# Kernel tuning notes

Hardware: AMD Instinct MI355X
Metric: run time of the kernel (lower is better)

Reference implementation:

```python
import jax, jax.numpy as jnp
import numpy as np

H = 4096        # hidden_size
NH = 32         # num query heads
NKV = 8         # num kv heads
HD = H // NH    # head_dim = 128
T_PREV = 16383  # cached tokens; new token makes T = 16384
BASE = 10000.0


def _rope(x, pos):
    # x: [heads, head_dim]; interleaved even/odd RoPE at a single position
    d = x.shape[-1]
    inv_freq = 1.0 / (BASE ** (jnp.arange(0, d, 2, dtype=jnp.float32) / d))
    f = pos * inv_freq                      # [d/2]
    c, s = jnp.cos(f), jnp.sin(f)
    xe, xo = x[..., 0::2], x[..., 1::2]
    out = jnp.stack([xe * c - xo * s, xe * s + xo * c], axis=-1)
    return out.reshape(x.shape)


def setup_inputs() -> dict:
    key = jax.random.key(0)
    ks = jax.random.split(key, 7)
    w = 0.02  # weight scale for numerical stability
    return {
        "hidden": jax.random.normal(ks[0], (H,), jnp.float32),
        "k_cache": jax.random.normal(ks[1], (T_PREV, NKV, HD), jnp.float32),
        "v_cache": jax.random.normal(ks[2], (T_PREV, NKV, HD), jnp.float32),
        "Wq": jax.random.normal(ks[3], (H, H), jnp.float32) * w,
        "Wk": jax.random.normal(ks[4], (NKV * HD, H), jnp.float32) * w,
        "Wv": jax.random.normal(ks[5], (NKV * HD, H), jnp.float32) * w,
        "Wo": jax.random.normal(ks[6], (H, H), jnp.float32) * w,
        "position_id": T_PREV,
    }


def reference(hidden, k_cache, v_cache, Wq, Wk, Wv, Wo, position_id):
    pos = jnp.float32(position_id)
    # projections (nn.Linear: y = W @ x), single token
    q = (Wq @ hidden).reshape(NH, HD)
    k = (Wk @ hidden).reshape(NKV, HD)
    v = (Wv @ hidden).reshape(NKV, HD)
    # inline RoPE on new q and k
    q = _rope(q, pos)
    k = _rope(k, pos)
    # contiguous KV including the new token
    k_all = jnp.concatenate([k_cache, k[None]], axis=0)   # [T, NKV, HD]
    v_all = jnp.concatenate([v_cache, v[None]], axis=0)
    # GQA: repeat KV heads to match query heads
    rep = NH // NKV
    k_all = jnp.repeat(k_all, rep, axis=1)                 # [T, NH, HD]
    v_all = jnp.repeat(v_all, rep, axis=1)
    # single-query attention
    scores = jnp.einsum('hd,thd->ht', q, k_all) / jnp.sqrt(jnp.float32(HD))
    attn = jax.nn.softmax(scores, axis=-1)                 # [NH, T]
    ctx = jnp.einsum('ht,thd->hd', attn, v_all)            # [NH, HD]
    # combine heads + output projection
    return Wo @ ctx.reshape(H)
```

## Files before the change

### kernel.cpp

```cpp
#include <hip/hip_runtime.h>
#include <math.h>
#include <stdint.h>

#define NH 32
#define NKV 8
#define HD 128
#define HDIM 4096
#define KVDIM 1024
#define TPREV 16383
#define NCHUNK 128
#define CHUNK 128
#define PTOK 64

#define OFF_Q 0
#define OFF_K 4096
#define OFF_V 5120
#define OFF_PART 6144
#define PART_STRIDE 132
#define OFF_CTX (OFF_PART + NH * NCHUNK * PART_STRIDE)

__device__ __forceinline__ float wave_reduce_sum(float v) {
#pragma unroll
  for (int m = 32; m >= 1; m >>= 1) v += __shfl_xor(v, m, 64);
  return v;
}
__device__ __forceinline__ float wave_reduce_max(float v) {
#pragma unroll
  for (int m = 32; m >= 1; m >>= 1) v = fmaxf(v, __shfl_xor(v, m, 64));
  return v;
}
__device__ __forceinline__ float dot4(float4 a, float4 b) {
  return a.x * b.x + a.y * b.y + a.z * b.z + a.w * b.w;
}

typedef const __attribute__((address_space(1))) unsigned int* gld_gp;
typedef __attribute__((address_space(3))) unsigned int* gld_lp;
__device__ __forceinline__ void cp16(const float* g, float* l) {
  __builtin_amdgcn_global_load_lds((gld_gp)(uintptr_t)g,
                                   (gld_lp)(uint32_t)(uintptr_t)l, 16, 0, 0);
}

#define BAR_LGKM()                                       \
  do {                                                   \
    asm volatile("s_waitcnt lgkmcnt(0)" ::: "memory");   \
    __builtin_amdgcn_s_barrier();                        \
    asm volatile("" ::: "memory");                       \
  } while (0)

__global__ __launch_bounds__(256) void qkv_rope_kernel(
    const float* __restrict__ Wq, const float* __restrict__ Wk,
    const float* __restrict__ Wv, const float* __restrict__ hidden,
    const int* __restrict__ pos_p, float* __restrict__ ws) {
  int r = blockIdx.x * 4 + (threadIdx.x >> 6);
  int lane = threadIdx.x & 63;
  const float* W;
  int wr;
  if (r < HDIM) {
    W = Wq; wr = r;
  } else if (r < HDIM + KVDIM) {
    W = Wk; wr = r - HDIM;
  } else {
    W = Wv; wr = r - HDIM - KVDIM;
  }
  const float4* w4 = (const float4*)(W + (size_t)wr * HDIM);
  const float4* h4 = (const float4*)hidden;
  float s = 0.f;
#pragma unroll
  for (int base = 0; base < 16; base += 8) {
    float4 a[8], b[8];
#pragma unroll
    for (int j = 0; j < 8; ++j) a[j] = w4[lane + 64 * (base + j)];
#pragma unroll
    for (int j = 0; j < 8; ++j) b[j] = h4[lane + 64 * (base + j)];
#pragma unroll
    for (int j = 0; j < 8; ++j) s += dot4(a[j], b[j]);
  }
  s = wave_reduce_sum(s);
  __shared__ float rs[4];
  if (lane == 0) rs[threadIdx.x >> 6] = s;
  __syncthreads();
  if (threadIdx.x < 2) {
    int r0 = blockIdx.x * 4 + (int)threadIdx.x * 2;
    float S0 = rs[threadIdx.x * 2], S1 = rs[threadIdx.x * 2 + 1];
    if (r0 < HDIM + KVDIM) {
      int j = (r0 & (HD - 1)) >> 1;
      double lowp = 1.0;
      if (j & 1) lowp *= 0.8659643233600653;
      if (j & 2) lowp *= 0.7498942093324559;
      if (j & 4) lowp *= 0.5623413251903491;
      if (j & 8) lowp *= 0.31622776601683794;
      double hi = (j & 16) ? 0.1 : 1.0;
      if (j & 32) hi *= 0.01;
      double f = (double)(*pos_p) * (lowp * hi);
      double k2 = floor(f * 0.15915494309189535);
      double rr = f - k2 * 6.283185307179586;
      float fr = (float)rr;
      float c = cosf(fr), sn = sinf(fr);
      ws[r0] = S0 * c - S1 * sn;
      ws[r0 + 1] = S0 * sn + S1 * c;
    } else {
      ws[r0] = S0;
      ws[r0 + 1] = S1;
    }
  }
}

__global__ __launch_bounds__(256, 2) void attn_chunk_kernel(
    const float* __restrict__ k_cache, const float* __restrict__ v_cache,
    float* __restrict__ ws) {
  int g = blockIdx.x >> 7;
  int c = blockIdx.x & 127;
  int t0 = c * CHUNK;
  int tid = threadIdx.x;
  int l = tid & 63, w = tid >> 6;

  __shared__ __align__(16) float Klds[PTOK * HD];
  __shared__ __align__(16) float Vlds[PTOK * HD];
  __shared__ __align__(16) float qs[4 * HD];
  __shared__ float sc[PTOK * 5];
  __shared__ float rm[4], rl[4], wold[4];
  __shared__ float wredm[4][4], wredl[4][4];

  if (tid < 4) { rm[tid] = -1e30f; rl[tid] = 0.f; }

  if (w < 2)
    cp16(ws + OFF_Q + (g << 9) + (w << 8) + (l << 2), qs + (w << 8));
#pragma unroll
  for (int i = 0; i < 8; ++i) {
    int tokA = (w << 4) + 2 * i;
    int toks = tokA + (l >> 5);
    int gt = t0 + toks;
    if (gt >= TPREV) gt = 0;
    cp16(k_cache + (size_t)gt * KVDIM + g * HD + (((l & 31) ^ (toks & 7)) << 2),
         Klds + (tokA << 7));
  }
#pragma unroll
  for (int i = 0; i < 8; ++i) {
    int tokA = (w << 4) + 2 * i;
    int toks = tokA + (l >> 5);
    int gt = t0 + toks;
    if (gt >= TPREV) gt = 0;
    cp16(v_cache + (size_t)gt * KVDIM + g * HD + ((l & 31) << 2),
         Vlds + (tokA << 7));
  }
  asm volatile("s_waitcnt vmcnt(8) lgkmcnt(0)" ::: "memory");
  __builtin_amdgcn_s_barrier();
  asm volatile("" ::: "memory");

  const float rscale = 0.08838834764831845f;
  int tokl = (w << 4) + (l & 15);
  int qq = l >> 4;
  int t7 = tokl & 7;
  int grp8 = tid >> 5, d4 = tid & 31;
  float4 acc0 = {0, 0, 0, 0}, acc1 = {0, 0, 0, 0};
  float4 acc2 = {0, 0, 0, 0}, acc3 = {0, 0, 0, 0};
  const float4* K4 = (const float4*)Klds;
  const float4* q4 = (const float4*)qs;
  const float4* V4 = (const float4*)Vlds;

#pragma unroll
  for (int p = 0; p < 2; ++p) {
    float s0 = 0.f, s1 = 0.f, s2 = 0.f, s3 = 0.f;
#pragma unroll
    for (int j = 0; j < 8; ++j) {
      float4 kk = K4[(tokl << 5) + (qq << 3) + (j ^ t7)];
      float4 qa = q4[0 * 32 + (qq << 3) + j];
      float4 qb = q4[1 * 32 + (qq << 3) + j];
      float4 qc = q4[2 * 32 + (qq << 3) + j];
      float4 qd_ = q4[3 * 32 + (qq << 3) + j];
      s0 += dot4(kk, qa); s1 += dot4(kk, qb);
      s2 += dot4(kk, qc); s3 += dot4(kk, qd_);
    }
    s0 += __shfl_xor(s0, 16, 64); s0 += __shfl_xor(s0, 32, 64);
    s1 += __shfl_xor(s1, 16, 64); s1 += __shfl_xor(s1, 32, 64);
    s2 += __shfl_xor(s2, 16, 64); s2 += __shfl_xor(s2, 32, 64);
    s3 += __shfl_xor(s3, 16, 64); s3 += __shfl_xor(s3, 32, 64);
    s0 *= rscale; s1 *= rscale; s2 *= rscale; s3 *= rscale;
    if (t0 + p * PTOK + tokl >= TPREV) {
      s0 = -1e30f; s1 = -1e30f; s2 = -1e30f; s3 = -1e30f;
    }

    float m0 = wave_reduce_max(s0), m1 = wave_reduce_max(s1);
    float m2 = wave_reduce_max(s2), m3 = wave_reduce_max(s3);
    if (l == 0) {
      wredm[w][0] = m0; wredm[w][1] = m1; wredm[w][2] = m2; wredm[w][3] = m3;
    }
    BAR_LGKM();
    if (p == 0) {
#pragma unroll
      for (int i = 0; i < 8; ++i) {
        int tokA = (w << 4) + 2 * i;
        int toks = tokA + (l >> 5);
        int gt = t0 + PTOK + toks;
        if (gt >= TPREV) gt = 0;
        cp16(k_cache + (size_t)gt * KVDIM + g * HD +
                 (((l & 31) ^ (toks & 7)) << 2),
             Klds + (tokA << 7));
      }
    }
    if (tid < 4) {
      float mh = fmaxf(fmaxf(wredm[0][tid], wredm[1][tid]),
                       fmaxf(wredm[2][tid], wredm[3][tid]));
      float M = fmaxf(rm[tid], mh);
      wold[tid] = expf(rm[tid] - M);
      rm[tid] = M;
    }
    BAR_LGKM();

    float M0 = rm[0], M1 = rm[1], M2 = rm[2], M3 = rm[3];
    float w0 = wold[0], w1 = wold[1], w2 = wold[2], w3 = wold[3];
    acc0.x *= w0; acc0.y *= w0; acc0.z *= w0; acc0.w *= w0;
    acc1.x *= w1; acc1.y *= w1; acc1.z *= w1; acc1.w *= w1;
    acc2.x *= w2; acc2.y *= w2; acc2.z *= w2; acc2.w *= w2;
    acc3.x *= w3; acc3.y *= w3; acc3.z *= w3; acc3.w *= w3;

    float e0 = expf(s0 - M0), e1 = expf(s1 - M1);
    float e2 = expf(s2 - M2), e3 = expf(s3 - M3);
    if (qq == 0) {
      sc[tokl * 5 + 0] = e0; sc[tokl * 5 + 1] = e1;
      sc[tokl * 5 + 2] = e2; sc[tokl * 5 + 3] = e3;
    }
    float l0 = 0.25f * wave_reduce_sum(e0), l1 = 0.25f * wave_reduce_sum(e1);
    float l2 = 0.25f * wave_reduce_sum(e2), l3 = 0.25f * wave_reduce_sum(e3);
    if (l == 0) {
      wredl[w][0] = l0; wredl[w][1] = l1; wredl[w][2] = l2; wredl[w][3] = l3;
    }
    if (p == 0)
      asm volatile("s_waitcnt vmcnt(8) lgkmcnt(0)" ::: "memory");
    else
      asm volatile("s_waitcnt vmcnt(0) lgkmcnt(0)" ::: "memory");
    __builtin_amdgcn_s_barrier();
    asm volatile("" ::: "memory");
    if (tid < 4)
      rl[tid] = rl[tid] * wold[tid] + wredl[0][tid] + wredl[1][tid] +
                wredl[2][tid] + wredl[3][tid];

#pragma unroll
    for (int t = 0; t < 8; ++t) {
      int tok = (grp8 << 3) + t;
      float4 vv = V4[(tok << 5) + d4];
      float p0_ = sc[tok * 5 + 0], p1_ = sc[tok * 5 + 1];
      float p2_ = sc[tok * 5 + 2], p3_ = sc[tok * 5 + 3];
      acc0.x = fmaf(p0_, vv.x, acc0.x); acc0.y = fmaf(p0_, vv.y, acc0.y);
      acc0.z = fmaf(p0_, vv.z, acc0.z); acc0.w = fmaf(p0_, vv.w, acc0.w);
      acc1.x = fmaf(p1_, vv.x, acc1.x); acc1.y = fmaf(p1_, vv.y, acc1.y);
      acc1.z = fmaf(p1_, vv.z, acc1.z); acc1.w = fmaf(p1_, vv.w, acc1.w);
      acc2.x = fmaf(p2_, vv.x, acc2.x); acc2.y = fmaf(p2_, vv.y, acc2.y);
      acc2.z = fmaf(p2_, vv.z, acc2.z); acc2.w = fmaf(p2_, vv.w, acc2.w);
      acc3.x = fmaf(p3_, vv.x, acc3.x); acc3.y = fmaf(p3_, vv.y, acc3.y);
      acc3.z = fmaf(p3_, vv.z, acc3.z); acc3.w = fmaf(p3_, vv.w, acc3.w);
    }

    if (p == 0) {
      BAR_LGKM();
#pragma unroll
      for (int i = 0; i < 8; ++i) {
        int tokA = (w << 4) + 2 * i;
        int toks = tokA + (l >> 5);
        int gt = t0 + PTOK + toks;
        if (gt >= TPREV) gt = 0;
        cp16(v_cache + (size_t)gt * KVDIM + g * HD + ((l & 31) << 2),
             Vlds + (tokA << 7));
      }
      asm volatile("s_waitcnt vmcnt(8)" ::: "memory");
    }
  }

  float4* vacc4 = (float4*)Klds;
  vacc4[(grp8 * 4 + 0) * 32 + d4] = acc0;
  vacc4[(grp8 * 4 + 1) * 32 + d4] = acc1;
  vacc4[(grp8 * 4 + 2) * 32 + d4] = acc2;
  vacc4[(grp8 * 4 + 3) * 32 + d4] = acc3;
  BAR_LGKM();
  if (tid < 128) {
    int h = tid >> 5, dd = tid & 31;
    float4 s = {0, 0, 0, 0};
#pragma unroll
    for (int g2 = 0; g2 < 8; ++g2) {
      float4 v = vacc4[(g2 * 4 + h) * 32 + dd];
      s.x += v.x; s.y += v.y; s.z += v.z; s.w += v.w;
    }
    float* dst = ws + OFF_PART +
                 ((size_t)(g * 4 + h) * NCHUNK + c) * PART_STRIDE + (dd << 2);
    *(float4*)dst = s;
  }
  if (tid < 4) {
    float* base =
        ws + OFF_PART + ((size_t)(g * 4 + tid) * NCHUNK + c) * PART_STRIDE;
    base[128] = rm[tid];
    base[129] = rl[tid];
  }
}

__global__ __launch_bounds__(256) void combine_kernel(float* __restrict__ ws) {
  int h = blockIdx.x;
  int g = h >> 2;
  int tid = threadIdx.x;
  const float rscale = 0.08838834764831845f;
  const float* ph = ws + OFF_PART + (size_t)h * NCHUNK * PART_STRIDE;

  __shared__ float red[HD];
  __shared__ float wexp[NCHUNK];
  __shared__ float wm[4], wl[4];
  __shared__ float acc2[HD];

  if (tid < HD) red[tid] = ws[OFF_Q + h * HD + tid] * ws[OFF_K + g * HD + tid];
  __syncthreads();
#pragma unroll
  for (int s2 = 64; s2 >= 1; s2 >>= 1) {
    if (tid < s2 && tid + s2 < HD) red[tid] += red[tid + s2];
    __syncthreads();
  }
  float snew = red[0] * rscale;

  float mv = (tid < NCHUNK) ? ph[(size_t)tid * PART_STRIDE + 128] : -1e30f;
  float lv = (tid < NCHUNK) ? ph[(size_t)tid * PART_STRIDE + 129] : 0.f;
  float mw = wave_reduce_max(mv);
  if ((tid & 63) == 0) wm[tid >> 6] = mw;
  __syncthreads();
  float M = fmaxf(fmaxf(fmaxf(wm[0], wm[1]), fmaxf(wm[2], wm[3])), snew);
  float w = expf(mv - M);
  if (tid < NCHUNK) wexp[tid] = w;
  float lw = wave_reduce_sum(lv * w);
  if ((tid & 63) == 0) wl[tid >> 6] = lw;
  __syncthreads();
  float en = expf(snew - M);
  float L = wl[0] + wl[1] + wl[2] + wl[3] + en;

  int half = tid >> 7, d = tid & 127;
  float acc = 0.f;
  int cbeg = half * (NCHUNK / 2);
#pragma unroll 8
  for (int c2 = cbeg; c2 < cbeg + NCHUNK / 2; ++c2)
    acc = fmaf(ph[(size_t)c2 * PART_STRIDE + d], wexp[c2], acc);
  if (half == 0) acc2[d] = acc;
  __syncthreads();
  if (half == 1) acc2[d] += acc;
  __syncthreads();
  if (tid < HD)
    ws[OFF_CTX + h * HD + tid] =
        (acc2[tid] + en * ws[OFF_V + g * HD + tid]) / L;
}

__global__ __launch_bounds__(256) void out_matvec_kernel(
    const float* __restrict__ Wo, const float* __restrict__ ws,
    float* __restrict__ out) {
  int r = blockIdx.x * 4 + (threadIdx.x >> 6);
  int lane = threadIdx.x & 63;
  const float4* w4 = (const float4*)(Wo + (size_t)r * HDIM);
  const float4* x4 = (const float4*)(ws + OFF_CTX);
  float s = 0.f;
#pragma unroll
  for (int base = 0; base < 16; base += 8) {
    float4 a[8], b[8];
#pragma unroll
    for (int j = 0; j < 8; ++j) a[j] = w4[lane + 64 * (base + j)];
#pragma unroll
    for (int j = 0; j < 8; ++j) b[j] = x4[lane + 64 * (base + j)];
#pragma unroll
    for (int j = 0; j < 8; ++j) s += dot4(a[j], b[j]);
  }
  s = wave_reduce_sum(s);
  if (lane == 0) out[r] = s;
}

extern "C" void kernel_launch(void* const* d_in, const int* in_sizes, int n_in,
                              void* d_out, int out_size, void* d_ws,
                              size_t ws_size, hipStream_t stream) {
  const float* hidden = (const float*)d_in[0];
  const float* k_cache = (const float*)d_in[1];
  const float* v_cache = (const float*)d_in[2];
  const float* Wq = (const float*)d_in[3];
  const float* Wk = (const float*)d_in[4];
  const float* Wv = (const float*)d_in[5];
  const float* Wo = (const float*)d_in[6];
  const int* pos = (const int*)d_in[7];
  float* out = (float*)d_out;
  float* ws = (float*)d_ws;

  qkv_rope_kernel<<<(HDIM + 2 * KVDIM) / 4, 256, 0, stream>>>(Wq, Wk, Wv,
                                                              hidden, pos, ws);
  attn_chunk_kernel<<<NKV * NCHUNK, 256, 0, stream>>>(k_cache, v_cache, ws);
  combine_kernel<<<NH, 256, 0, stream>>>(ws);
  out_matvec_kernel<<<HDIM / 4, 256, 0, stream>>>(Wo, ws, out);
}
```

Baseline: 287.1 us.

## Split attention into 64-token chunks with single-pass softmax and direct V loads

Halves the chunk size to 64 tokens and doubles the number of chunk blocks, so each block computes one chunk's scores and softmax in a single pass with no online rescaling or double-buffered K/V. V is now read straight from global memory into registers instead of being staged through LDS, which drops the V shared buffer and raises the occupancy target to 4 blocks per CU. The combine kernel now reads 256 per-chunk partials (one per thread). The trade-off is twice as many partial results to write and combine, and the loss of K/V load overlap inside each block.

```diff
diff --git a/kernel.cpp b/kernel.cpp
--- a/kernel.cpp
+++ b/kernel.cpp
@@ -8,9 +8,8 @@
 #define HDIM 4096
 #define KVDIM 1024
 #define TPREV 16383
-#define NCHUNK 128
-#define CHUNK 128
-#define PTOK 64
+#define NCHUNK 256
+#define CHUNK 64
 
 #define OFF_Q 0
 #define OFF_K 4096
@@ -39,13 +38,6 @@
   __builtin_amdgcn_global_load_lds((gld_gp)(uintptr_t)g,
                                    (gld_lp)(uint32_t)(uintptr_t)l, 16, 0, 0);
 }
-
-#define BAR_LGKM()                                       \
-  do {                                                   \
-    asm volatile("s_waitcnt lgkmcnt(0)" ::: "memory");   \
-    __builtin_amdgcn_s_barrier();                        \
-    asm volatile("" ::: "memory");                       \
-  } while (0)
 
 __global__ __launch_bounds__(256) void qkv_rope_kernel(
     const float* __restrict__ Wq, const float* __restrict__ Wk,
@@ -105,23 +97,19 @@
   }
 }
 
-__global__ __launch_bounds__(256, 2) void attn_chunk_kernel(
+__global__ __launch_bounds__(256, 4) void attn_chunk_kernel(
     const float* __restrict__ k_cache, const float* __restrict__ v_cache,
     float* __restrict__ ws) {
-  int g = blockIdx.x >> 7;
-  int c = blockIdx.x & 127;
+  int g = blockIdx.x >> 8;
+  int c = blockIdx.x & 255;
   int t0 = c * CHUNK;
   int tid = threadIdx.x;
   int l = tid & 63, w = tid >> 6;
 
-  __shared__ __align__(16) float Klds[PTOK * HD];
-  __shared__ __align__(16) float Vlds[PTOK * HD];
+  __shared__ __align__(16) float Klds[CHUNK * HD];
   __shared__ __align__(16) float qs[4 * HD];
-  __shared__ float sc[PTOK * 5];
-  __shared__ float rm[4], rl[4], wold[4];
+  __shared__ float sc[CHUNK * 5];
   __shared__ float wredm[4][4], wredl[4][4];
-
-  if (tid < 4) { rm[tid] = -1e30f; rl[tid] = 0.f; }
 
   if (w < 2)
     cp16(ws + OFF_Q + (g << 9) + (w << 8) + (l << 2), qs + (w << 8));
@@ -134,144 +122,99 @@
     cp16(k_cache + (size_t)gt * KVDIM + g * HD + (((l & 31) ^ (toks & 7)) << 2),
          Klds + (tokA << 7));
   }
-#pragma unroll
-  for (int i = 0; i < 8; ++i) {
-    int tokA = (w << 4) + 2 * i;
-    int toks = tokA + (l >> 5);
-    int gt = t0 + toks;
-    if (gt >= TPREV) gt = 0;
-    cp16(v_cache + (size_t)gt * KVDIM + g * HD + ((l & 31) << 2),
-         Vlds + (tokA << 7));
-  }
-  asm volatile("s_waitcnt vmcnt(8) lgkmcnt(0)" ::: "memory");
-  __builtin_amdgcn_s_barrier();
-  asm volatile("" ::: "memory");
+  __syncthreads();
 
   const float rscale = 0.08838834764831845f;
   int tokl = (w << 4) + (l & 15);
   int qq = l >> 4;
   int t7 = tokl & 7;
-  int grp8 = tid >> 5, d4 = tid & 31;
+  const float4* K4 = (const float4*)Klds;
+  const float4* q4 = (const float4*)qs;
+  float s0 = 0.f, s1 = 0.f, s2 = 0.f, s3 = 0.f;
+#pragma unroll
+  for (int j = 0; j < 8; ++j) {
+    float4 kk = K4[(tokl << 5) + (qq << 3) + (j ^ t7)];
+    float4 qa = q4[0 * 32 + (qq << 3) + j];
+    float4 qb = q4[1 * 32 + (qq << 3) + j];
+    float4 qc = q4[2 * 32 + (qq << 3) + j];
+    float4 qd_ = q4[3 * 32 + (qq << 3) + j];
+    s0 += dot4(kk, qa); s1 += dot4(kk, qb);
+    s2 += dot4(kk, qc); s3 += dot4(kk, qd_);
+  }
+  s0 += __shfl_xor(s0, 16, 64); s0 += __shfl_xor(s0, 32, 64);
+  s1 += __shfl_xor(s1, 16, 64); s1 += __shfl_xor(s1, 32, 64);
+  s2 += __shfl_xor(s2, 16, 64); s2 += __shfl_xor(s2, 32, 64);
+  s3 += __shfl_xor(s3, 16, 64); s3 += __shfl_xor(s3, 32, 64);
+  s0 *= rscale; s1 *= rscale; s2 *= rscale; s3 *= rscale;
+  if (t0 + tokl >= TPREV) {
+    s0 = -1e30f; s1 = -1e30f; s2 = -1e30f; s3 = -1e30f;
+  }
+
+  float m0 = wave_reduce_max(s0), m1 = wave_reduce_max(s1);
+  float m2 = wave_reduce_max(s2), m3 = wave_reduce_max(s3);
+  if (l == 0) {
+    wredm[w][0] = m0; wredm[w][1] = m1; wredm[w][2] = m2; wredm[w][3] = m3;
+  }
+  __syncthreads();
+  float mh0 = fmaxf(fmaxf(wredm[0][0], wredm[1][0]),
+                    fmaxf(wredm[2][0], wredm[3][0]));
+  float mh1 = fmaxf(fmaxf(wredm[0][1], wredm[1][1]),
+                    fmaxf(wredm[2][1], wredm[3][1]));
+  float mh2 = fmaxf(fmaxf(wredm[0][2], wredm[1][2]),
+                    fmaxf(wredm[2][2], wredm[3][2]));
+  float mh3 = fmaxf(fmaxf(wredm[0][3], wredm[1][3]),
+                    fmaxf(wredm[2][3], wredm[3][3]));
+
+  float e0 = expf(s0 - mh0), e1 = expf(s1 - mh1);
+  float e2 = expf(s2 - mh2), e3 = expf(s3 - mh3);
+  if (qq == 0) {
+    sc[tokl * 5 + 0] = e0; sc[tokl * 5 + 1] = e1;
+    sc[tokl * 5 + 2] = e2; sc[tokl * 5 + 3] = e3;
+  }
+  float l0 = 0.25f * wave_reduce_sum(e0), l1 = 0.25f * wave_reduce_sum(e1);
+  float l2 = 0.25f * wave_reduce_sum(e2), l3 = 0.25f * wave_reduce_sum(e3);
+  if (l == 0) {
+    wredl[w][0] = l0; wredl[w][1] = l1; wredl[w][2] = l2; wredl[w][3] = l3;
+  }
+  __syncthreads();
+
+  int grp = tid >> 5, d4 = tid & 31;
   float4 acc0 = {0, 0, 0, 0}, acc1 = {0, 0, 0, 0};
   float4 acc2 = {0, 0, 0, 0}, acc3 = {0, 0, 0, 0};
-  const float4* K4 = (const float4*)Klds;
-  const float4* q4 = (const float4*)qs;
-  const float4* V4 = (const float4*)Vlds;
-
-#pragma unroll
-  for (int p = 0; p < 2; ++p) {
-    float s0 = 0.f, s1 = 0.f, s2 = 0.f, s3 = 0.f;
-#pragma unroll
-    for (int j = 0; j < 8; ++j) {
-      float4 kk = K4[(tokl << 5) + (qq << 3) + (j ^ t7)];
-      float4 qa = q4[0 * 32 + (qq << 3) + j];
-      float4 qb = q4[1 * 32 + (qq << 3) + j];
-      float4 qc = q4[2 * 32 + (qq << 3) + j];
-      float4 qd_ = q4[3 * 32 + (qq << 3) + j];
-      s0 += dot4(kk, qa); s1 += dot4(kk, qb);
-      s2 += dot4(kk, qc); s3 += dot4(kk, qd_);
+  const float4 z4 = {0, 0, 0, 0};
+#pragma unroll
+  for (int base = 0; base < 8; base += 4) {
+    float4 vv[4];
+#pragma unroll
+    for (int j = 0; j < 4; ++j) {
+      int it = grp + 8 * (base + j);
+      int t = t0 + it;
+      vv[j] = (t < TPREV)
+                  ? ((const float4*)(v_cache + (size_t)t * KVDIM + g * HD))[d4]
+                  : z4;
     }
-    s0 += __shfl_xor(s0, 16, 64); s0 += __shfl_xor(s0, 32, 64);
-    s1 += __shfl_xor(s1, 16, 64); s1 += __shfl_xor(s1, 32, 64);
-    s2 += __shfl_xor(s2, 16, 64); s2 += __shfl_xor(s2, 32, 64);
-    s3 += __shfl_xor(s3, 16, 64); s3 += __shfl_xor(s3, 32, 64);
-    s0 *= rscale; s1 *= rscale; s2 *= rscale; s3 *= rscale;
-    if (t0 + p * PTOK + tokl >= TPREV) {
-      s0 = -1e30f; s1 = -1e30f; s2 = -1e30f; s3 = -1e30f;
+#pragma unroll
+    for (int j = 0; j < 4; ++j) {
+      int it = grp + 8 * (base + j);
+      float p0 = sc[it * 5 + 0], p1 = sc[it * 5 + 1];
+      float p2 = sc[it * 5 + 2], p3 = sc[it * 5 + 3];
+      acc0.x = fmaf(p0, vv[j].x, acc0.x); acc0.y = fmaf(p0, vv[j].y, acc0.y);
+      acc0.z = fmaf(p0, vv[j].z, acc0.z); acc0.w = fmaf(p0, vv[j].w, acc0.w);
+      acc1.x = fmaf(p1, vv[j].x, acc1.x); acc1.y = fmaf(p1, vv[j].y, acc1.y);
+      acc1.z = fmaf(p1, vv[j].z, acc1.z); acc1.w = fmaf(p1, vv[j].w, acc1.w);
+      acc2.x = fmaf(p2, vv[j].x, acc2.x); acc2.y = fmaf(p2, vv[j].y, acc2.y);
+      acc2.z = fmaf(p2, vv[j].z, acc2.z); acc2.w = fmaf(p2, vv[j].w, acc2.w);
+      acc3.x = fmaf(p3, vv[j].x, acc3.x); acc3.y = fmaf(p3, vv[j].y, acc3.y);
+      acc3.z = fmaf(p3, vv[j].z, acc3.z); acc3.w = fmaf(p3, vv[j].w, acc3.w);
     }
-
-    float m0 = wave_reduce_max(s0), m1 = wave_reduce_max(s1);
-    float m2 = wave_reduce_max(s2), m3 = wave_reduce_max(s3);
-    if (l == 0) {
-      wredm[w][0] = m0; wredm[w][1] = m1; wredm[w][2] = m2; wredm[w][3] = m3;
-    }
-    BAR_LGKM();
-    if (p == 0) {
-#pragma unroll
-      for (int i = 0; i < 8; ++i) {
-        int tokA = (w << 4) + 2 * i;
-        int toks = tokA + (l >> 5);
-        int gt = t0 + PTOK + toks;
-        if (gt >= TPREV) gt = 0;
-        cp16(k_cache + (size_t)gt * KVDIM + g * HD +
-                 (((l & 31) ^ (toks & 7)) << 2),
-             Klds + (tokA << 7));
-      }
-    }
-    if (tid < 4) {
-      float mh = fmaxf(fmaxf(wredm[0][tid], wredm[1][tid]),
-                       fmaxf(wredm[2][tid], wredm[3][tid]));
-      float M = fmaxf(rm[tid], mh);
-      wold[tid] = expf(rm[tid] - M);
-      rm[tid] = M;
-    }
-    BAR_LGKM();
-
-    float M0 = rm[0], M1 = rm[1], M2 = rm[2], M3 = rm[3];
-    float w0 = wold[0], w1 = wold[1], w2 = wold[2], w3 = wold[3];
-    acc0.x *= w0; acc0.y *= w0; acc0.z *= w0; acc0.w *= w0;
-    acc1.x *= w1; acc1.y *= w1; acc1.z *= w1; acc1.w *= w1;
-    acc2.x *= w2; acc2.y *= w2; acc2.z *= w2; acc2.w *= w2;
-    acc3.x *= w3; acc3.y *= w3; acc3.z *= w3; acc3.w *= w3;
-
-    float e0 = expf(s0 - M0), e1 = expf(s1 - M1);
-    float e2 = expf(s2 - M2), e3 = expf(s3 - M3);
-    if (qq == 0) {
-      sc[tokl * 5 + 0] = e0; sc[tokl * 5 + 1] = e1;
-      sc[tokl * 5 + 2] = e2; sc[tokl * 5 + 3] = e3;
-    }
-    float l0 = 0.25f * wave_reduce_sum(e0), l1 = 0.25f * wave_reduce_sum(e1);
-    float l2 = 0.25f * wave_reduce_sum(e2), l3 = 0.25f * wave_reduce_sum(e3);
-    if (l == 0) {
-      wredl[w][0] = l0; wredl[w][1] = l1; wredl[w][2] = l2; wredl[w][3] = l3;
-    }
-    if (p == 0)
-      asm volatile("s_waitcnt vmcnt(8) lgkmcnt(0)" ::: "memory");
-    else
-      asm volatile("s_waitcnt vmcnt(0) lgkmcnt(0)" ::: "memory");
-    __builtin_amdgcn_s_barrier();
-    asm volatile("" ::: "memory");
-    if (tid < 4)
-      rl[tid] = rl[tid] * wold[tid] + wredl[0][tid] + wredl[1][tid] +
-                wredl[2][tid] + wredl[3][tid];
-
-#pragma unroll
-    for (int t = 0; t < 8; ++t) {
-      int tok = (grp8 << 3) + t;
-      float4 vv = V4[(tok << 5) + d4];
-      float p0_ = sc[tok * 5 + 0], p1_ = sc[tok * 5 + 1];
-      float p2_ = sc[tok * 5 + 2], p3_ = sc[tok * 5 + 3];
-      acc0.x = fmaf(p0_, vv.x, acc0.x); acc0.y = fmaf(p0_, vv.y, acc0.y);
-      acc0.z = fmaf(p0_, vv.z, acc0.z); acc0.w = fmaf(p0_, vv.w, acc0.w);
-      acc1.x = fmaf(p1_, vv.x, acc1.x); acc1.y = fmaf(p1_, vv.y, acc1.y);
-      acc1.z = fmaf(p1_, vv.z, acc1.z); acc1.w = fmaf(p1_, vv.w, acc1.w);
-      acc2.x = fmaf(p2_, vv.x, acc2.x); acc2.y = fmaf(p2_, vv.y, acc2.y);
-      acc2.z = fmaf(p2_, vv.z, acc2.z); acc2.w = fmaf(p2_, vv.w, acc2.w);
-      acc3.x = fmaf(p3_, vv.x, acc3.x); acc3.y = fmaf(p3_, vv.y, acc3.y);
-      acc3.z = fmaf(p3_, vv.z, acc3.z); acc3.w = fmaf(p3_, vv.w, acc3.w);
-    }
-
-    if (p == 0) {
-      BAR_LGKM();
-#pragma unroll
-      for (int i = 0; i < 8; ++i) {
-        int tokA = (w << 4) + 2 * i;
-        int toks = tokA + (l >> 5);
-        int gt = t0 + PTOK + toks;
-        if (gt >= TPREV) gt = 0;
-        cp16(v_cache + (size_t)gt * KVDIM + g * HD + ((l & 31) << 2),
-             Vlds + (tokA << 7));
-      }
-      asm volatile("s_waitcnt vmcnt(8)" ::: "memory");
-    }
-  }
-
+  }
   float4* vacc4 = (float4*)Klds;
-  vacc4[(grp8 * 4 + 0) * 32 + d4] = acc0;
-  vacc4[(grp8 * 4 + 1) * 32 + d4] = acc1;
-  vacc4[(grp8 * 4 + 2) * 32 + d4] = acc2;
-  vacc4[(grp8 * 4 + 3) * 32 + d4] = acc3;
-  BAR_LGKM();
+  vacc4[(grp * 4 + 0) * 32 + d4] = acc0;
+  vacc4[(grp * 4 + 1) * 32 + d4] = acc1;
+  vacc4[(grp * 4 + 2) * 32 + d4] = acc2;
+  vacc4[(grp * 4 + 3) * 32 + d4] = acc3;
+  __syncthreads();
+
   if (tid < 128) {
     int h = tid >> 5, dd = tid & 31;
     float4 s = {0, 0, 0, 0};
@@ -285,10 +228,13 @@
     *(float4*)dst = s;
   }
   if (tid < 4) {
+    float mh = fmaxf(fmaxf(wredm[0][tid], wredm[1][tid]),
+                     fmaxf(wredm[2][tid], wredm[3][tid]));
+    float lh = wredl[0][tid] + wredl[1][tid] + wredl[2][tid] + wredl[3][tid];
     float* base =
         ws + OFF_PART + ((size_t)(g * 4 + tid) * NCHUNK + c) * PART_STRIDE;
-    base[128] = rm[tid];
-    base[129] = rl[tid];
+    base[128] = mh;
+    base[129] = lh;
   }
 }
 
@@ -313,14 +259,14 @@
   }
   float snew = red[0] * rscale;
 
-  float mv = (tid < NCHUNK) ? ph[(size_t)tid * PART_STRIDE + 128] : -1e30f;
-  float lv = (tid < NCHUNK) ? ph[(size_t)tid * PART_STRIDE + 129] : 0.f;
+  float mv = ph[(size_t)tid * PART_STRIDE + 128];
+  float lv = ph[(size_t)tid * PART_STRIDE + 129];
   float mw = wave_reduce_max(mv);
   if ((tid & 63) == 0) wm[tid >> 6] = mw;
   __syncthreads();
   float M = fmaxf(fmaxf(fmaxf(wm[0], wm[1]), fmaxf(wm[2], wm[3])), snew);
   float w = expf(mv - M);
-  if (tid < NCHUNK) wexp[tid] = w;
+  wexp[tid] = w;
   float lw = wave_reduce_sum(lv * w);
   if ((tid & 63) == 0) wl[tid >> 6] = lw;
   __syncthreads();
```

After: 292.5 us. About the same (+1.9%).
